# Kernel optimization log

Hardware: AMD Instinct MI355X
Metric: run time of the kernel (lower is better)

## Reference

```python
import jax, jax.numpy as jnp
import numpy as np

L, H, D, DH, F = 2, 12, 768, 64, 3072
B, T = 2, 2048
LN_EPS = 1e-5


def setup_inputs() -> dict:
    key = jax.random.key(0)
    ks = jax.random.split(key, 16)
    s = 0.02
    inp = {
        "x": jax.random.normal(ks[0], (B, T, D), dtype=jnp.float32),
        "attn_mask": jnp.ones((1, T, T), dtype=jnp.int32),
        # per-layer, per-head QKV projections
        "Wq": jax.random.normal(ks[1], (L, H, D, DH), jnp.float32) * s,
        "bq": jnp.zeros((L, H, DH), jnp.float32),
        "Wk": jax.random.normal(ks[2], (L, H, D, DH), jnp.float32) * s,
        "bk": jnp.zeros((L, H, DH), jnp.float32),
        "Wv": jax.random.normal(ks[3], (L, H, D, DH), jnp.float32) * s,
        "bv": jnp.zeros((L, H, DH), jnp.float32),
        # output projection over concatenated heads
        "Wo": jax.random.normal(ks[4], (L, H * DH, D), jnp.float32) * s,
        "bo": jnp.zeros((L, D), jnp.float32),
        # FFN: LayerNorm -> Linear -> GELU -> Linear
        "ln_g": jnp.ones((L, D), jnp.float32),
        "ln_b": jnp.zeros((L, D), jnp.float32),
        "W1": jax.random.normal(ks[5], (L, D, F), jnp.float32) * s,
        "b1": jnp.zeros((L, F), jnp.float32),
        "W2": jax.random.normal(ks[6], (L, F, D), jnp.float32) * s,
        "b2": jnp.zeros((L, D), jnp.float32),
    }
    return inp


def _layer(x, mask, Wq, bq, Wk, bk, Wv, bv, Wo, bo, ln_g, ln_b, W1, b1, W2, b2):
    # batched multi-head attention (equivalent to per-head loop in source)
    q = jnp.einsum("btd,hde->bhte", x, Wq) + bq[None, :, None, :]
    k = jnp.einsum("btd,hde->bhte", x, Wk) + bk[None, :, None, :]
    v = jnp.einsum("btd,hde->bhte", x, Wv) + bv[None, :, None, :]
    scores = jnp.einsum("bhte,bhse->bhts", q, k) / np.sqrt(DH).astype(np.float32)
    scores = jnp.where(mask[:, None, :, :] == 0, -jnp.inf, scores)
    alpha = jax.nn.softmax(scores, axis=-1)
    attn = jnp.einsum("bhts,bhse->bhte", alpha, v)  # [B,H,T,DH]
    concat = attn.transpose(0, 2, 1, 3).reshape(x.shape[0], x.shape[1], H * DH)
    x = concat @ Wo + bo + x  # attention residual
    # FFN with pre-LayerNorm inside the block, residual around it
    mu = jnp.mean(x, axis=-1, keepdims=True)
    var = jnp.mean(jnp.square(x - mu), axis=-1, keepdims=True)
    h = (x - mu) * jax.lax.rsqrt(var + LN_EPS) * ln_g + ln_b
    h = jax.nn.gelu(h @ W1 + b1, approximate=False) @ W2 + b2
    return h + x


def reference(x, attn_mask, Wq, bq, Wk, bk, Wv, bv, Wo, bo, ln_g, ln_b, W1, b1, W2, b2):
    for l in range(L):
        x = _layer(x, attn_mask,
                   Wq[l], bq[l], Wk[l], bk[l], Wv[l], bv[l],
                   Wo[l], bo[l], ln_g[l], ln_b[l],
                   W1[l], b1[l], W2[l], b2[l])
    return x
```

## Files before the change

kernel.cpp:

```cpp
#include <hip/hip_runtime.h>
#include <math.h>

#define CL 2
#define CH 12
#define CD 768
#define CDH 64
#define CF 3072
#define CB 2
#define CT 2048
#define CBH (CB * CH)
#define CBTCD ((size_t)CB * CT * CD)

typedef __bf16 bf16x8 __attribute__((ext_vector_type(8)));
typedef float f32x4 __attribute__((ext_vector_type(4)));
typedef short s16x4 __attribute__((ext_vector_type(4)));
typedef ushort u16x4 __attribute__((ext_vector_type(4)));

#define QSCALE 0.18033688011112042f

__device__ __forceinline__ ushort f2bf(float f) {
  return __builtin_bit_cast(ushort, (__bf16)f);
}

__device__ __forceinline__ float fexp2(float x) {
  float r;
  asm volatile("v_exp_f32 %0, %1" : "=v"(r) : "v"(x));
  return r;
}

__device__ __forceinline__ float wred_sum(float v) {
#pragma unroll
  for (int o = 32; o > 0; o >>= 1) v += __shfl_xor(v, o);
  return v;
}

__device__ __forceinline__ void gload16(const ushort* g, ushort* l) {
  __builtin_amdgcn_global_load_lds(
      (const __attribute__((address_space(1))) unsigned int*)g,
      (__attribute__((address_space(3))) unsigned int*)l, 16, 0, 0);
}

enum { EPI_BF16 = 1, EPI_BIAS_BF16 = 2, EPI_BIAS_GELU_BF16 = 3, EPI_BIAS_RES_F32 = 4, EPI_BIAS_RES_F32_BF16 = 5, EPI_PART_F32 = 6, EPI_QKV = 7 };

template <int EPI>
__global__ __launch_bounds__(256) void gemm_k(
    const ushort* __restrict__ A, int lda,
    const ushort* __restrict__ B, int ldb,
    void* __restrict__ Cv, int ldc,
    int K,
    const float* __restrict__ bias,
    const float* __restrict__ res,
    ushort* __restrict__ C2) {
  __shared__ ushort As[3][128 * 32];
  __shared__ ushort Bs[3][128 * 32];
  const int tid = threadIdx.x;
  const int lane = tid & 63;
  const int wave = tid >> 6;
  const int wm = (wave >> 1) * 64;
  const int wn = (wave & 1) * 64;

  const int gx = gridDim.x;
  const int nwg = gx * gridDim.y;
  int wgid = blockIdx.y * gx + blockIdx.x;
  const int cpx = nwg >> 3;
  wgid = (wgid & 7) * cpx + (wgid >> 3);
  const int m0 = (wgid / gx) * 128;
  const int n0 = (wgid % gx) * 128;

  const int lr = lane & 15;
  const int lg = lane >> 4;
  f32x4 acc[4][4] = {};

  const int kz = blockIdx.z * K;
  const ushort* pa = A + (size_t)(m0 + (tid >> 2)) * lda + (tid & 3) * 8 + kz;
  const ushort* pb = B + (size_t)(n0 + (tid >> 2)) * ldb + (tid & 3) * 8 + kz;

  auto stage = [&](int buf, int k0) {
#pragma unroll
    for (int p = 0; p < 2; ++p) {
      gload16(pa + (size_t)p * 64 * lda + k0, &As[buf][wave * 512 + p * 2048]);
      gload16(pb + (size_t)p * 64 * ldb + k0, &Bs[buf][wave * 512 + p * 2048]);
    }
  };

  const int nt = K >> 5;
  stage(0, 0);
  stage(1, 32);
  for (int kt = 0; kt < nt; ++kt) {
    const int cur = kt % 3;
    if (kt + 2 < nt) {
      stage((kt + 2) % 3, (kt + 2) << 5);
      asm volatile("s_waitcnt vmcnt(8)" ::: "memory");
    } else if (kt + 1 < nt) {
      asm volatile("s_waitcnt vmcnt(4)" ::: "memory");
    } else {
      asm volatile("s_waitcnt vmcnt(0)" ::: "memory");
    }
    __builtin_amdgcn_s_barrier();
    __builtin_amdgcn_sched_barrier(0);

    bf16x8 af[4], bfr[4];
#pragma unroll
    for (int f = 0; f < 4; ++f) af[f] = *(const bf16x8*)(&As[cur][(wm + f * 16 + lr) * 32 + lg * 8]);
#pragma unroll
    for (int f = 0; f < 4; ++f) bfr[f] = *(const bf16x8*)(&Bs[cur][(wn + f * 16 + lr) * 32 + lg * 8]);
#pragma unroll
    for (int i = 0; i < 4; ++i)
#pragma unroll
      for (int j = 0; j < 4; ++j)
        acc[i][j] = __builtin_amdgcn_mfma_f32_16x16x32_bf16(af[i], bfr[j], acc[i][j], 0, 0, 0);

    __builtin_amdgcn_sched_barrier(0);
    __builtin_amdgcn_s_barrier();
  }

  const int cr0 = lg * 4;
#pragma unroll
  for (int i = 0; i < 4; ++i) {
#pragma unroll
    for (int j = 0; j < 4; ++j) {
      int col = n0 + wn + j * 16 + lr;
      if constexpr (EPI == EPI_QKV) {
        const int cbase = n0 + wn + j * 16;
        const int row0 = m0 + wm + i * 16 + cr0;
        float bcol = bias[col];
        if (cbase >= 2 * CD) {
          const int bb = row0 >> 11;
          const int t0 = row0 & (CT - 1);
          const int hh = (cbase - 2 * CD) >> 6;
          const int ee = ((cbase - 2 * CD) & 63) + lr;
          u16x4 o;
#pragma unroll
          for (int r = 0; r < 4; ++r) o[r] = f2bf(acc[i][j][r] + bcol);
          *(u16x4*)(C2 + ((size_t)(bb * CH + hh) * 64 + ee) * CT + t0) = o;
        } else {
#pragma unroll
          for (int r = 0; r < 4; ++r)
            ((ushort*)Cv)[(size_t)(row0 + r) * ldc + col] = f2bf(acc[i][j][r] + bcol);
        }
        continue;
      }
#pragma unroll
      for (int r = 0; r < 4; ++r) {
        int row = m0 + wm + i * 16 + cr0 + r;
        float val = acc[i][j][r];
        size_t offc = (size_t)row * ldc + col;
        if constexpr (EPI == EPI_BF16) {
          ((ushort*)Cv)[offc] = f2bf(val);
        } else if constexpr (EPI == EPI_BIAS_BF16) {
          ((ushort*)Cv)[offc] = f2bf(val + bias[col]);
        } else if constexpr (EPI == EPI_BIAS_GELU_BF16) {
          float x = val + bias[col];
          float gel = 0.5f * x * (1.0f + erff(x * 0.70710678118654752f));
          ((ushort*)Cv)[offc] = f2bf(gel);
        } else if constexpr (EPI == EPI_BIAS_RES_F32) {
          ((float*)Cv)[offc] = val + bias[col] + res[offc];
        } else if constexpr (EPI == EPI_PART_F32) {
          ((float*)Cv)[blockIdx.z * CBTCD + offc] = val;
        } else if constexpr (EPI == EPI_BIAS_RES_F32_BF16) {
          float o = val + bias[col] + res[offc];
          ((float*)Cv)[offc] = o;
          C2[offc] = f2bf(o);
        }
      }
    }
  }
}

template <bool DUAL>
__global__ __launch_bounds__(256) void reduce2_k(const float* __restrict__ part,
                                                 const float* __restrict__ bias,
                                                 const float* __restrict__ res,
                                                 float* __restrict__ outf,
                                                 ushort* __restrict__ outb) {
  int i = blockIdx.x * 256 + threadIdx.x;
  float4 p0 = ((const float4*)part)[i];
  float4 p1 = ((const float4*)(part + CBTCD))[i];
  float4 rr = ((const float4*)res)[i];
  int col = (i * 4) % CD;
  float4 bb = *(const float4*)(bias + col);
  float4 o;
  o.x = p0.x + p1.x + rr.x + bb.x;
  o.y = p0.y + p1.y + rr.y + bb.y;
  o.z = p0.z + p1.z + rr.z + bb.z;
  o.w = p0.w + p1.w + rr.w + bb.w;
  ((float4*)outf)[i] = o;
  if constexpr (DUAL) {
    ushort4 u;
    u.x = f2bf(o.x); u.y = f2bf(o.y); u.z = f2bf(o.z); u.w = f2bf(o.w);
    ((ushort4*)outb)[i] = u;
  }
}

__global__ __launch_bounds__(256) void flash_k(const ushort* __restrict__ qkv,
                                               const ushort* __restrict__ vt,
                                               const unsigned* __restrict__ mbits,
                                               ushort* __restrict__ out) {
  const int q0 = blockIdx.x * 64;
  const int bh = blockIdx.y;
  const int b = bh / CH, h = bh % CH;
  const int tid = threadIdx.x;
  const int lane = tid & 63;
  const int wave = tid >> 6;
  const int lr = lane & 15;
  const int lg = lane >> 4;

  __shared__ ushort Ks[64][72];
  __shared__ ushort Vt[64][72];

  const int qg = q0 + wave * 16 + lr;
  const ushort* qrow = qkv + ((size_t)(b * CT) + qg) * 2304 + h * CDH;
  bf16x8 aq0 = *(const bf16x8*)(qrow + lg * 8);
  bf16x8 aq1 = *(const bf16x8*)(qrow + 32 + lg * 8);

  f32x4 acc[4] = {};
  float m_run = -1e30f, l_run = 0.f;

  const ushort* kbase = qkv + (size_t)(b * CT) * 2304 + CD + h * CDH;
  const ushort* vbase = vt + (size_t)bh * 64 * CT;

  const int r0 = tid >> 3, r1 = 32 + (tid >> 3), cc = (tid & 7) * 8;

  auto ld = [&](int kv0, bf16x8& k0, bf16x8& k1, bf16x8& v0, bf16x8& v1) {
    k0 = *(const bf16x8*)(kbase + (size_t)(kv0 + r0) * 2304 + cc);
    k1 = *(const bf16x8*)(kbase + (size_t)(kv0 + r1) * 2304 + cc);
    v0 = *(const bf16x8*)(vbase + (size_t)r0 * CT + kv0 + cc);
    v1 = *(const bf16x8*)(vbase + (size_t)r1 * CT + kv0 + cc);
  };
  auto st = [&](bf16x8 k0, bf16x8 k1, bf16x8 v0, bf16x8 v1) {
    *(bf16x8*)(&Ks[r0][cc]) = k0;
    *(bf16x8*)(&Ks[r1][cc]) = k1;
    *(bf16x8*)(&Vt[r0][cc]) = v0;
    *(bf16x8*)(&Vt[r1][cc]) = v1;
  };

  auto compute = [&](int kv0) {
    f32x4 stt[4];
    __builtin_amdgcn_s_setprio(1);
#pragma unroll
    for (int j = 0; j < 4; ++j) {
      bf16x8 kf0 = *(const bf16x8*)(&Ks[j * 16 + lr][lg * 8]);
      bf16x8 kf1 = *(const bf16x8*)(&Ks[j * 16 + lr][32 + lg * 8]);
      f32x4 t = {};
      t = __builtin_amdgcn_mfma_f32_16x16x32_bf16(kf0, aq0, t, 0, 0, 0);
      t = __builtin_amdgcn_mfma_f32_16x16x32_bf16(kf1, aq1, t, 0, 0, 0);
      stt[j] = t;
    }
    __builtin_amdgcn_s_setprio(0);

    unsigned w0 = mbits[(size_t)qg * 64 + (kv0 >> 5)];
    unsigned w1 = mbits[(size_t)qg * 64 + (kv0 >> 5) + 1];
    float tmax = -INFINITY;
    if ((w0 & w1) == 0xFFFFFFFFu) {
#pragma unroll
      for (int j = 0; j < 4; ++j)
#pragma unroll
        for (int r = 0; r < 4; ++r) tmax = fmaxf(tmax, stt[j][r]);
    } else {
#pragma unroll
      for (int j = 0; j < 4; ++j) {
        unsigned w = (j < 2) ? w0 : w1;
#pragma unroll
        for (int r = 0; r < 4; ++r) {
          int bit = (j * 16 + lg * 4 + r) & 31;
          if (((w >> bit) & 1u) == 0u) stt[j][r] = -INFINITY;
          tmax = fmaxf(tmax, stt[j][r]);
        }
      }
    }
    tmax = fmaxf(tmax, __shfl_xor(tmax, 16));
    tmax = fmaxf(tmax, __shfl_xor(tmax, 32));

    if (__any(tmax - m_run > 8.0f)) {
      float mnew = fmaxf(m_run, tmax);
      float sc = fexp2(m_run - mnew);
      m_run = mnew;
      l_run *= sc;
#pragma unroll
      for (int jj = 0; jj < 4; ++jj) {
        acc[jj][0] *= sc; acc[jj][1] *= sc; acc[jj][2] *= sc; acc[jj][3] *= sc;
      }
    }

    s16x4 pf[4];
#pragma unroll
    for (int j = 0; j < 4; ++j) {
      s16x4 pv;
#pragma unroll
      for (int r = 0; r < 4; ++r) {
        float p = fexp2(stt[j][r] - m_run);
        l_run += p;
        pv[r] = (short)f2bf(p);
      }
      pf[j] = pv;
    }

    __builtin_amdgcn_s_setprio(1);
#pragma unroll
    for (int jj = 0; jj < 4; ++jj) {
#pragma unroll
      for (int j = 0; j < 4; ++j) {
        s16x4 vf = *(const s16x4*)(&Vt[jj * 16 + lr][j * 16 + lg * 4]);
        acc[jj] = __builtin_amdgcn_mfma_f32_16x16x16bf16_1k(vf, pf[j], acc[jj], 0, 0, 0);
      }
    }
    __builtin_amdgcn_s_setprio(0);
  };

  bf16x8 ka0, ka1, va0, va1, kb0, kb1, vb0, vb1;
  ld(0, ka0, ka1, va0, va1);
  for (int kv0 = 0; kv0 < CT; kv0 += 128) {
    __syncthreads();
    st(ka0, ka1, va0, va1);
    __syncthreads();
    ld(kv0 + 64, kb0, kb1, vb0, vb1);
    compute(kv0);
    __syncthreads();
    st(kb0, kb1, vb0, vb1);
    __syncthreads();
    if (kv0 + 128 < CT) ld(kv0 + 128, ka0, ka1, va0, va1);
    compute(kv0 + 64);
  }

  l_run += __shfl_xor(l_run, 16);
  l_run += __shfl_xor(l_run, 32);

  float inv = 1.0f / l_run;
  const int orow = b * CT + qg;
#pragma unroll
  for (int jj = 0; jj < 4; ++jj) {
    u16x4 o;
#pragma unroll
    for (int r = 0; r < 4; ++r) o[r] = f2bf(acc[jj][r] * inv);
    *(u16x4*)(out + (size_t)orow * CD + h * CDH + jj * 16 + lg * 4) = o;
  }
}

__global__ void maskbits_k(const int* __restrict__ mask, unsigned* __restrict__ mbits) {
  int idx = blockIdx.x * 256 + threadIdx.x;
  if (idx >= CT * 64) return;
  const int* mp = mask + (size_t)(idx >> 6) * CT + (idx & 63) * 32;
  unsigned bits = 0;
#pragma unroll
  for (int j = 0; j < 32; ++j) bits |= (mp[j] != 0 ? 1u : 0u) << j;
  mbits[idx] = bits;
}

__global__ __launch_bounds__(256) void ln_k(const float* __restrict__ X,
                                            ushort* __restrict__ H,
                                            const float* __restrict__ g,
                                            const float* __restrict__ b) {
  const int t = blockIdx.x;
  const int tid = threadIdx.x;
  const float* row = X + (size_t)t * CD;
  float x0 = row[tid], x1 = row[tid + 256], x2 = row[tid + 512];
  float s = wred_sum(x0 + x1 + x2);
  __shared__ float sh[4], sh2[4];
  if ((tid & 63) == 0) sh[tid >> 6] = s;
  __syncthreads();
  float mu = (sh[0] + sh[1] + sh[2] + sh[3]) * (1.0f / 768.0f);
  float d0 = x0 - mu, d1 = x1 - mu, d2 = x2 - mu;
  float vs = wred_sum(d0 * d0 + d1 * d1 + d2 * d2);
  if ((tid & 63) == 0) sh2[tid >> 6] = vs;
  __syncthreads();
  float var = (sh2[0] + sh2[1] + sh2[2] + sh2[3]) * (1.0f / 768.0f);
  float r = 1.0f / sqrtf(var + 1e-5f);
  H[(size_t)t * CD + tid] = f2bf(d0 * r * g[tid] + b[tid]);
  H[(size_t)t * CD + tid + 256] = f2bf(d1 * r * g[tid + 256] + b[tid + 256]);
  H[(size_t)t * CD + tid + 512] = f2bf(d2 * r * g[tid + 512] + b[tid + 512]);
}

__global__ void f32_to_bf16_k(const float* __restrict__ in, ushort* __restrict__ out, int n4) {
  int i = blockIdx.x * 256 + threadIdx.x;
  if (i >= n4) return;
  float4 f = *(const float4*)(in + (size_t)i * 4);
  ushort4 u;
  u.x = f2bf(f.x); u.y = f2bf(f.y); u.z = f2bf(f.z); u.w = f2bf(f.w);
  *(ushort4*)(out + (size_t)i * 4) = u;
}

__global__ __launch_bounds__(256) void tcvt_k(const float* __restrict__ src, size_t sbs,
                                              ushort* __restrict__ dst, size_t dbs,
                                              int R, int C, float scale) {
  __shared__ float t[32][33];
  const float* s = src + blockIdx.z * sbs;
  ushort* d = dst + blockIdx.z * dbs;
  const int tx = threadIdx.x & 31;
  const int ty4 = (threadIdx.x >> 5) * 4;
  const int r0 = blockIdx.y * 32, c0 = blockIdx.x * 32;
#pragma unroll
  for (int i = 0; i < 4; ++i) t[ty4 + i][tx] = s[(size_t)(r0 + ty4 + i) * C + c0 + tx];
  __syncthreads();
#pragma unroll
  for (int i = 0; i < 4; ++i)
    d[(size_t)(c0 + ty4 + i) * R + r0 + tx] = f2bf(t[tx][ty4 + i] * scale);
}

__global__ void repack_bqkv_k(const float* __restrict__ bq, const float* __restrict__ bk,
                              const float* __restrict__ bv, float* __restrict__ dst) {
  int idx = blockIdx.x * 256 + threadIdx.x;
  if (idx >= CL * 2304) return;
  int l = idx / 2304;
  int c = idx % 2304;
  int sec = c / CD;
  int within = c % CD;
  int h = within / CDH;
  int e = within % CDH;
  const float* B = (sec == 0) ? bq : ((sec == 1) ? bk : bv);
  float v = B[((size_t)l * CH + h) * CDH + e];
  if (sec == 0) v *= QSCALE;
  dst[idx] = v;
}

extern "C" void kernel_launch(void* const* d_in, const int* in_sizes, int n_in,
                              void* d_out, int out_size, void* d_ws, size_t ws_size,
                              hipStream_t stream) {
  (void)in_sizes; (void)n_in; (void)out_size; (void)ws_size;
  const float* X = (const float*)d_in[0];
  const int* MSK = (const int*)d_in[1];
  const float* Wq = (const float*)d_in[2];
  const float* bq = (const float*)d_in[3];
  const float* Wk = (const float*)d_in[4];
  const float* bk = (const float*)d_in[5];
  const float* Wv = (const float*)d_in[6];
  const float* bv = (const float*)d_in[7];
  const float* Wo = (const float*)d_in[8];
  const float* bo = (const float*)d_in[9];
  const float* lng = (const float*)d_in[10];
  const float* lnb = (const float*)d_in[11];
  const float* W1 = (const float*)d_in[12];
  const float* b1 = (const float*)d_in[13];
  const float* W2 = (const float*)d_in[14];
  const float* b2 = (const float*)d_in[15];

  char* base = (char*)d_ws;
  size_t off = 0;
  auto alloc = [&](size_t bytes) {
    char* p = base + off;
    off = (off + bytes + 255) & ~(size_t)255;
    return p;
  };
  ushort* wqkv_t = (ushort*)alloc((size_t)CL * 2304 * CD * 2);
  ushort* wo_t = (ushort*)alloc((size_t)CL * CD * CD * 2);
  ushort* w1_t = (ushort*)alloc((size_t)CL * CF * CD * 2);
  ushort* w2_t = (ushort*)alloc((size_t)CL * CD * CF * 2);
  float* bqkv = (float*)alloc((size_t)CL * 2304 * 4);
  ushort* xb = (ushort*)alloc((size_t)CB * CT * CD * 2);
  ushort* qkv = (ushort*)alloc((size_t)CB * CT * 2304 * 2);
  ushort* vt = (ushort*)alloc((size_t)CB * CH * CDH * CT * 2);
  unsigned* mbits = (unsigned*)alloc((size_t)CT * 64 * 4);
  ushort* attno = (ushort*)alloc((size_t)CB * CT * CD * 2);
  float* xattn = (float*)alloc((size_t)CB * CT * CD * 4);
  float* xf = (float*)alloc((size_t)CB * CT * CD * 4);
  ushort* hln = (ushort*)alloc((size_t)CB * CT * CD * 2);
  ushort* gbuf = (ushort*)alloc((size_t)CB * CT * CF * 2);
  float* part = (float*)qkv;

  const int BT_ = CB * CT;

  for (int l = 0; l < CL; ++l) {
    tcvt_k<<<dim3(CDH / 32, CD / 32, CH), 256, 0, stream>>>(
        Wq + (size_t)l * CH * CD * CDH, (size_t)CD * CDH,
        wqkv_t + (size_t)l * 2304 * CD + 0 * CD * CD, (size_t)CDH * CD,
        CD, CDH, QSCALE);
    tcvt_k<<<dim3(CDH / 32, CD / 32, CH), 256, 0, stream>>>(
        Wk + (size_t)l * CH * CD * CDH, (size_t)CD * CDH,
        wqkv_t + (size_t)l * 2304 * CD + 1 * CD * CD, (size_t)CDH * CD,
        CD, CDH, 1.0f);
    tcvt_k<<<dim3(CDH / 32, CD / 32, CH), 256, 0, stream>>>(
        Wv + (size_t)l * CH * CD * CDH, (size_t)CD * CDH,
        wqkv_t + (size_t)l * 2304 * CD + 2 * CD * CD, (size_t)CDH * CD,
        CD, CDH, 1.0f);
  }
  tcvt_k<<<dim3(CD / 32, CD / 32, CL), 256, 0, stream>>>(
      Wo, (size_t)CD * CD, wo_t, (size_t)CD * CD, CD, CD, 1.0f);
  tcvt_k<<<dim3(CF / 32, CD / 32, CL), 256, 0, stream>>>(
      W1, (size_t)CD * CF, w1_t, (size_t)CF * CD, CD, CF, 1.0f);
  tcvt_k<<<dim3(CD / 32, CF / 32, CL), 256, 0, stream>>>(
      W2, (size_t)CF * CD, w2_t, (size_t)CD * CF, CF, CD, 1.0f);
  {
    int n = CL * 2304;
    repack_bqkv_k<<<(n + 255) / 256, 256, 0, stream>>>(bq, bk, bv, bqkv);
  }
  maskbits_k<<<(CT * 64 + 255) / 256, 256, 0, stream>>>(MSK, mbits);

  {
    int n4 = BT_ * CD / 4;
    f32_to_bf16_k<<<(n4 + 255) / 256, 256, 0, stream>>>(X, xb, n4);
  }

  for (int l = 0; l < CL; ++l) {
    const float* xcur = (l == 0) ? X : xf;
    gemm_k<EPI_QKV><<<dim3(2304 / 128, BT_ / 128), 256, 0, stream>>>(
        xb, CD, wqkv_t + (size_t)l * 2304 * CD, CD, qkv, 2304, CD,
        bqkv + (size_t)l * 2304, nullptr, vt);
    flash_k<<<dim3(CT / 64, CBH), 256, 0, stream>>>(qkv, vt, mbits, attno);
    gemm_k<EPI_BIAS_RES_F32><<<dim3(CD / 128, BT_ / 128), 256, 0, stream>>>(
        attno, CD, wo_t + (size_t)l * CD * CD, CD, xattn, CD, CD,
        bo + (size_t)l * CD, xcur, nullptr);
    ln_k<<<BT_, 256, 0, stream>>>(xattn, hln, lng + (size_t)l * CD, lnb + (size_t)l * CD);
    gemm_k<EPI_BIAS_GELU_BF16><<<dim3(CF / 128, BT_ / 128), 256, 0, stream>>>(
        hln, CD, w1_t + (size_t)l * CF * CD, CD, gbuf, CF, CD,
        b1 + (size_t)l * CF, nullptr, nullptr);
    gemm_k<EPI_PART_F32><<<dim3(CD / 128, BT_ / 128, 2), 256, 0, stream>>>(
        gbuf, CF, w2_t + (size_t)l * CD * CF, CF, part, CD, CF / 2,
        nullptr, nullptr, nullptr);
    const int nred = BT_ * CD / 4 / 256;
    if (l == CL - 1) {
      reduce2_k<false><<<nred, 256, 0, stream>>>(part, b2 + (size_t)l * CD, xattn,
                                                 (float*)d_out, nullptr);
    } else {
      reduce2_k<true><<<nred, 256, 0, stream>>>(part, b2 + (size_t)l * CD, xattn,
                                                xf, xb);
    }
  }
}
```

Baseline: 431.7 us.

## Double-buffer K/V shared tiles in flash attention with one barrier per tile

The flash attention kernel's shared K and V tiles become two ping-pong buffers. Global loads now prefetch two tiles ahead, and the loop needs one lightweight barrier (lgkmcnt wait plus s_barrier) per 64-key tile instead of two __syncthreads. This cuts synchronisation stalls and lets the LDS stores of the next tile overlap with MFMA work on the current one. It doubles the LDS footprint and keeps more prefetch registers live, which could lower occupancy.

```diff
diff --git a/kernel.cpp b/kernel.cpp
--- a/kernel.cpp
+++ b/kernel.cpp
@@ -205,8 +205,8 @@
   const int lr = lane & 15;
   const int lg = lane >> 4;
 
-  __shared__ ushort Ks[64][72];
-  __shared__ ushort Vt[64][72];
+  __shared__ ushort Ks[2][64][72];
+  __shared__ ushort Vt[2][64][72];
 
   const int qg = q0 + wave * 16 + lr;
   const ushort* qrow = qkv + ((size_t)(b * CT) + qg) * 2304 + h * CDH;
@@ -227,20 +227,25 @@
     v0 = *(const bf16x8*)(vbase + (size_t)r0 * CT + kv0 + cc);
     v1 = *(const bf16x8*)(vbase + (size_t)r1 * CT + kv0 + cc);
   };
-  auto st = [&](bf16x8 k0, bf16x8 k1, bf16x8 v0, bf16x8 v1) {
-    *(bf16x8*)(&Ks[r0][cc]) = k0;
-    *(bf16x8*)(&Ks[r1][cc]) = k1;
-    *(bf16x8*)(&Vt[r0][cc]) = v0;
-    *(bf16x8*)(&Vt[r1][cc]) = v1;
+  auto st = [&](int buf, bf16x8 k0, bf16x8 k1, bf16x8 v0, bf16x8 v1) {
+    *(bf16x8*)(&Ks[buf][r0][cc]) = k0;
+    *(bf16x8*)(&Ks[buf][r1][cc]) = k1;
+    *(bf16x8*)(&Vt[buf][r0][cc]) = v0;
+    *(bf16x8*)(&Vt[buf][r1][cc]) = v1;
   };
-
-  auto compute = [&](int kv0) {
+  auto bar = [&]() {
+    asm volatile("s_waitcnt lgkmcnt(0)" ::: "memory");
+    __builtin_amdgcn_s_barrier();
+    __builtin_amdgcn_sched_barrier(0);
+  };
+
+  auto compute = [&](int kv0, int buf) {
     f32x4 stt[4];
     __builtin_amdgcn_s_setprio(1);
 #pragma unroll
     for (int j = 0; j < 4; ++j) {
-      bf16x8 kf0 = *(const bf16x8*)(&Ks[j * 16 + lr][lg * 8]);
-      bf16x8 kf1 = *(const bf16x8*)(&Ks[j * 16 + lr][32 + lg * 8]);
+      bf16x8 kf0 = *(const bf16x8*)(&Ks[buf][j * 16 + lr][lg * 8]);
+      bf16x8 kf1 = *(const bf16x8*)(&Ks[buf][j * 16 + lr][32 + lg * 8]);
       f32x4 t = {};
       t = __builtin_amdgcn_mfma_f32_16x16x32_bf16(kf0, aq0, t, 0, 0, 0);
       t = __builtin_amdgcn_mfma_f32_16x16x32_bf16(kf1, aq1, t, 0, 0, 0);
@@ -300,26 +305,29 @@
     for (int jj = 0; jj < 4; ++jj) {
 #pragma unroll
       for (int j = 0; j < 4; ++j) {
-        s16x4 vf = *(const s16x4*)(&Vt[jj * 16 + lr][j * 16 + lg * 4]);
+        s16x4 vf = *(const s16x4*)(&Vt[buf][jj * 16 + lr][j * 16 + lg * 4]);
         acc[jj] = __builtin_amdgcn_mfma_f32_16x16x16bf16_1k(vf, pf[j], acc[jj], 0, 0, 0);
       }
     }
     __builtin_amdgcn_s_setprio(0);
   };
 
-  bf16x8 ka0, ka1, va0, va1, kb0, kb1, vb0, vb1;
-  ld(0, ka0, ka1, va0, va1);
-  for (int kv0 = 0; kv0 < CT; kv0 += 128) {
-    __syncthreads();
-    st(ka0, ka1, va0, va1);
-    __syncthreads();
-    ld(kv0 + 64, kb0, kb1, vb0, vb1);
-    compute(kv0);
-    __syncthreads();
-    st(kb0, kb1, vb0, vb1);
-    __syncthreads();
-    if (kv0 + 128 < CT) ld(kv0 + 128, ka0, ka1, va0, va1);
-    compute(kv0 + 64);
+  bf16x8 kx0, kx1, vx0, vx1, ky0, ky1, vy0, vy1;
+  ld(0, kx0, kx1, vx0, vx1);
+  ld(64, ky0, ky1, vy0, vy1);
+  st(0, kx0, kx1, vx0, vx1);
+  bar();
+  for (int t = 0; t < 32; t += 2) {
+    if (t + 2 < 32) ld((t + 2) * 64, kx0, kx1, vx0, vx1);
+    compute(t * 64, 0);
+    st(1, ky0, ky1, vy0, vy1);
+    bar();
+    if (t + 3 < 32) ld((t + 3) * 64, ky0, ky1, vy0, vy1);
+    compute((t + 1) * 64, 1);
+    if (t + 2 < 32) {
+      st(0, kx0, kx1, vx0, vx1);
+      bar();
+    }
   }
 
   l_run += __shfl_xor(l_run, 16);
```

Measured after the change: 431.4 us. No clear change (-0.1%).
